# Kernel tuning notes

Hardware: AMD Instinct MI355X
Metric: run time of the kernel (lower is better)

The kernel has to match this reference:

```python
import jax, jax.numpy as jnp
import numpy as np

B, NX, NR, D, H = 8, 512, 512, 256, 256


def setup_inputs() -> dict:
    key = jax.random.key(0)
    ks = jax.random.split(key, 8)
    s = 1.0 / np.sqrt(D)
    sh = 1.0 / np.sqrt(H)
    return {
        "X": jax.random.normal(ks[0], (B, NX, D), dtype=jnp.float32),
        "ref": jax.random.normal(ks[1], (B, NR, D), dtype=jnp.float32),
        "W_X": jax.random.normal(ks[2], (H, D), dtype=jnp.float32) * s,
        "b_X": jax.random.normal(ks[3], (H,), dtype=jnp.float32) * s,
        "W_ref": jax.random.normal(ks[4], (H, D), dtype=jnp.float32) * s,
        "b_ref": jax.random.normal(ks[5], (H,), dtype=jnp.float32) * s,
        "v_w": jax.random.normal(ks[6], (1, H), dtype=jnp.float32) * sh,
        "v_b": jax.random.normal(ks[7], (1,), dtype=jnp.float32) * sh,
    }


def reference(X, ref, W_X, b_X, W_ref, b_ref, v_w, v_b):
    # linear projections: [B, nX, H], [B, nR, H]
    hX = jnp.einsum('bxd,hd->bxh', X, W_X) + b_X
    hR = jnp.einsum('brd,hd->brh', ref, W_ref) + b_ref
    # additive (Bahdanau) scores: [B, nX, nR]
    t = jnp.tanh(hX[:, :, None, :] + hR[:, None, :, :])
    out = jnp.einsum('bxrh,h->bxr', t, v_w[0]) + v_b[0]
    # softmax over the n_X axis (dim=1 in torch)
    attn = jax.nn.softmax(out, axis=1)
    # weighted sum of X per ref position: [B, nR, D]
    weighted_X = jnp.einsum('bxe,bxr->bre', X, attn)
    return weighted_X
```

## Files before the change

### kernel.cpp

```cpp
#include <hip/hip_runtime.h>
#include <math.h>

#define CB 8
#define CNX 512
#define CNR 512
#define CD 256
#define CH 256

typedef __attribute__((ext_vector_type(8))) short short8;
typedef __attribute__((ext_vector_type(4))) float f32x4;

__device__ __forceinline__ float fast_rcp(float x) {
#if __has_builtin(__builtin_amdgcn_rcpf)
  return __builtin_amdgcn_rcpf(x);
#else
  return 1.0f / x;
#endif
}
__device__ __forceinline__ float fast_exp2(float x) {
#if __has_builtin(__builtin_amdgcn_exp2f)
  return __builtin_amdgcn_exp2f(x);
#else
  return exp2f(x);
#endif
}

__device__ __forceinline__ void cvt_store(unsigned short* dstH,
                                          unsigned short* dstL,
                                          float4 v0, float4 v1) {
  unsigned u0x = __float_as_uint(v0.x), u0y = __float_as_uint(v0.y);
  unsigned u0z = __float_as_uint(v0.z), u0w = __float_as_uint(v0.w);
  unsigned u1x = __float_as_uint(v1.x), u1y = __float_as_uint(v1.y);
  unsigned u1z = __float_as_uint(v1.z), u1w = __float_as_uint(v1.w);
  uint4 H;
  H.x = (u0x >> 16) | (u0y & 0xFFFF0000u);
  H.y = (u0z >> 16) | (u0w & 0xFFFF0000u);
  H.z = (u1x >> 16) | (u1y & 0xFFFF0000u);
  H.w = (u1z >> 16) | (u1w & 0xFFFF0000u);
  float r0x = v0.x - __uint_as_float(u0x & 0xFFFF0000u);
  float r0y = v0.y - __uint_as_float(u0y & 0xFFFF0000u);
  float r0z = v0.z - __uint_as_float(u0z & 0xFFFF0000u);
  float r0w = v0.w - __uint_as_float(u0w & 0xFFFF0000u);
  float r1x = v1.x - __uint_as_float(u1x & 0xFFFF0000u);
  float r1y = v1.y - __uint_as_float(u1y & 0xFFFF0000u);
  float r1z = v1.z - __uint_as_float(u1z & 0xFFFF0000u);
  float r1w = v1.w - __uint_as_float(u1w & 0xFFFF0000u);
  uint4 L;
  L.x = (__float_as_uint(r0x) >> 16) | (__float_as_uint(r0y) & 0xFFFF0000u);
  L.y = (__float_as_uint(r0z) >> 16) | (__float_as_uint(r0w) & 0xFFFF0000u);
  L.z = (__float_as_uint(r1x) >> 16) | (__float_as_uint(r1y) & 0xFFFF0000u);
  L.w = (__float_as_uint(r1z) >> 16) | (__float_as_uint(r1w) & 0xFFFF0000u);
  *(uint4*)dstH = H;
  *(uint4*)dstL = L;
}

__device__ __forceinline__ void split4(float4 v, ushort4* H, ushort4* L) {
  unsigned ux = __float_as_uint(v.x), uy = __float_as_uint(v.y);
  unsigned uz = __float_as_uint(v.z), uw = __float_as_uint(v.w);
  H->x = (unsigned short)(ux >> 16);
  H->y = (unsigned short)(uy >> 16);
  H->z = (unsigned short)(uz >> 16);
  H->w = (unsigned short)(uw >> 16);
  float rx = v.x - __uint_as_float(ux & 0xFFFF0000u);
  float ry = v.y - __uint_as_float(uy & 0xFFFF0000u);
  float rz = v.z - __uint_as_float(uz & 0xFFFF0000u);
  float rw = v.w - __uint_as_float(uw & 0xFFFF0000u);
  L->x = (unsigned short)(__float_as_uint(rx) >> 16);
  L->y = (unsigned short)(__float_as_uint(ry) >> 16);
  L->z = (unsigned short)(__float_as_uint(rz) >> 16);
  L->w = (unsigned short)(__float_as_uint(rw) >> 16);
}

__global__ __launch_bounds__(256) void proj_mfma(
    const float* __restrict__ A0, const float* __restrict__ A1,
    const float* __restrict__ W0, const float* __restrict__ W1,
    const float* __restrict__ bias0, const float* __restrict__ bias1,
    float* __restrict__ E0, float* __restrict__ E1) {
  __shared__ unsigned short lds[2][4][64][40];
  const int K = CD;
  int z = blockIdx.z;
  const float* A = z ? A1 : A0;
  const float* W = z ? W1 : W0;
  const float* bias = z ? bias1 : bias0;
  float* ET = z ? E1 : E0;
  int m0 = blockIdx.x * 64, n0 = blockIdx.y * 64;
  int tid = threadIdx.x;
  int lane = tid & 63, w = tid >> 6;
  int wm = w >> 1, wn = w & 1;
  int r = tid >> 2, kq = (tid & 3) * 8;
  const float* pA = A + (size_t)(m0 + r) * K + kq;
  const float* pW = W + (size_t)(n0 + r) * K + kq;
  f32x4 acc[2][2] = {};
  float4 a0 = *(const float4*)(pA);
  float4 a1 = *(const float4*)(pA + 4);
  float4 w0 = *(const float4*)(pW);
  float4 w1 = *(const float4*)(pW + 4);
  cvt_store(&lds[0][0][r][kq], &lds[0][1][r][kq], a0, a1);
  cvt_store(&lds[0][2][r][kq], &lds[0][3][r][kq], w0, w1);
  for (int s = 0; s < 8; s++) {
    __syncthreads();
    if (s < 7) {
      int kt = (s + 1) * 32;
      a0 = *(const float4*)(pA + kt);
      a1 = *(const float4*)(pA + kt + 4);
      w0 = *(const float4*)(pW + kt);
      w1 = *(const float4*)(pW + kt + 4);
    }
    int cur = s & 1;
    int arow = wm * 32 + (lane & 15);
    int brow = wn * 32 + (lane & 15);
    int koff = (lane >> 4) * 8;
    short8 ah0 = *(const short8*)&lds[cur][0][arow][koff];
    short8 ah1 = *(const short8*)&lds[cur][0][arow + 16][koff];
    short8 al0 = *(const short8*)&lds[cur][1][arow][koff];
    short8 al1 = *(const short8*)&lds[cur][1][arow + 16][koff];
    short8 bh0 = *(const short8*)&lds[cur][2][brow][koff];
    short8 bh1 = *(const short8*)&lds[cur][2][brow + 16][koff];
    short8 bl0 = *(const short8*)&lds[cur][3][brow][koff];
    short8 bl1 = *(const short8*)&lds[cur][3][brow + 16][koff];
    acc[0][0] = __builtin_amdgcn_mfma_f32_16x16x32_bf16(ah0, bh0, acc[0][0], 0, 0, 0);
    acc[0][1] = __builtin_amdgcn_mfma_f32_16x16x32_bf16(ah0, bh1, acc[0][1], 0, 0, 0);
    acc[1][0] = __builtin_amdgcn_mfma_f32_16x16x32_bf16(ah1, bh0, acc[1][0], 0, 0, 0);
    acc[1][1] = __builtin_amdgcn_mfma_f32_16x16x32_bf16(ah1, bh1, acc[1][1], 0, 0, 0);
    acc[0][0] = __builtin_amdgcn_mfma_f32_16x16x32_bf16(ah0, bl0, acc[0][0], 0, 0, 0);
    acc[0][1] = __builtin_amdgcn_mfma_f32_16x16x32_bf16(ah0, bl1, acc[0][1], 0, 0, 0);
    acc[1][0] = __builtin_amdgcn_mfma_f32_16x16x32_bf16(ah1, bl0, acc[1][0], 0, 0, 0);
    acc[1][1] = __builtin_amdgcn_mfma_f32_16x16x32_bf16(ah1, bl1, acc[1][1], 0, 0, 0);
    acc[0][0] = __builtin_amdgcn_mfma_f32_16x16x32_bf16(al0, bh0, acc[0][0], 0, 0, 0);
    acc[0][1] = __builtin_amdgcn_mfma_f32_16x16x32_bf16(al0, bh1, acc[0][1], 0, 0, 0);
    acc[1][0] = __builtin_amdgcn_mfma_f32_16x16x32_bf16(al1, bh0, acc[1][0], 0, 0, 0);
    acc[1][1] = __builtin_amdgcn_mfma_f32_16x16x32_bf16(al1, bh1, acc[1][1], 0, 0, 0);
    if (s < 7) {
      int nxt = cur ^ 1;
      cvt_store(&lds[nxt][0][r][kq], &lds[nxt][1][r][kq], a0, a1);
      cvt_store(&lds[nxt][2][r][kq], &lds[nxt][3][r][kq], w0, w1);
    }
  }
  const float K2L = 2.8853900817779268f;
  int b = m0 >> 9;
  int xq = (m0 & 511) + wm * 32 + (lane >> 4) * 4;
#pragma unroll
  for (int mi = 0; mi < 2; mi++) {
#pragma unroll
    for (int ni = 0; ni < 2; ni++) {
      int h = n0 + wn * 32 + ni * 16 + (lane & 15);
      float bb = bias[h];
      f32x4 a = acc[mi][ni];
      float4 o = {fast_exp2(K2L * (a[0] + bb)), fast_exp2(K2L * (a[1] + bb)),
                  fast_exp2(K2L * (a[2] + bb)), fast_exp2(K2L * (a[3] + bb))};
      *(float4*)(ET + ((size_t)b * CH + h) * CNX + xq + mi * 16) = o;
    }
  }
}

__global__ __launch_bounds__(512) void scores_kernel(
    const float* __restrict__ exT, const float* __restrict__ erT,
    const float* __restrict__ v_w, float* __restrict__ scT) {
  __shared__ float smem[4 * 2048 + 256];
  int b = blockIdx.z;
  int x0 = blockIdx.x * 64, r0 = blockIdx.y * 64;
  int tid = threadIdx.x;
  int g = tid >> 8;
  int t = tid & 255;
  float* xs = smem + g * 4096;
  float* rs = xs + 2048;
  float* vsh = smem + 8192;
  if (tid < 256) vsh[tid] = v_w[tid];
  int tx = t & 15, ty = t >> 4;
  int sr = t >> 4, sc = (t & 15) * 4;
  int wrot = (tid >> 6) & 7;
  const float* pX = exT + (size_t)b * CH * CNX + x0 + sc;
  const float* pR = erT + (size_t)b * CH * CNR + r0 + sc;
  int hb = g * 32;
  float4 xa0 = *(const float4*)(pX + (size_t)(hb + sr) * CNX);
  float4 xa1 = *(const float4*)(pX + (size_t)(hb + sr + 16) * CNX);
  float4 ra0 = *(const float4*)(pR + (size_t)(hb + sr) * CNR);
  float4 ra1 = *(const float4*)(pR + (size_t)(hb + sr + 16) * CNR);
  float acc[4][4] = {};
  for (int hc = hb; hc < CH; hc += 64) {
    __syncthreads();
    *(float4*)&xs[sr * 64 + sc] = xa0;
    *(float4*)&xs[(sr + 16) * 64 + sc] = xa1;
    *(float4*)&rs[sr * 64 + sc] = ra0;
    *(float4*)&rs[(sr + 16) * 64 + sc] = ra1;
    __syncthreads();
    if (hc + 64 < CH) {
      xa0 = *(const float4*)(pX + (size_t)(hc + 64 + sr) * CNX);
      xa1 = *(const float4*)(pX + (size_t)(hc + 64 + sr + 16) * CNX);
      ra0 = *(const float4*)(pR + (size_t)(hc + 64 + sr) * CNR);
      ra1 = *(const float4*)(pR + (size_t)(hc + 64 + sr + 16) * CNR);
    }
#pragma unroll 2
    for (int hq = 0; hq < 8; hq++) {
      int h0 = ((hq + wrot) & 7) * 4;
      float4 vv = *(const float4*)&vsh[hc + h0];
      float4 xv0 = *(const float4*)&xs[(h0 + 0) * 64 + tx * 4];
      float4 xv1 = *(const float4*)&xs[(h0 + 1) * 64 + tx * 4];
      float4 xv2 = *(const float4*)&xs[(h0 + 2) * 64 + tx * 4];
      float4 xv3 = *(const float4*)&xs[(h0 + 3) * 64 + tx * 4];
      float4 rv0 = *(const float4*)&rs[(h0 + 0) * 64 + ty * 4];
      float4 rv1 = *(const float4*)&rs[(h0 + 1) * 64 + ty * 4];
      float4 rv2 = *(const float4*)&rs[(h0 + 2) * 64 + ty * 4];
      float4 rv3 = *(const float4*)&rs[(h0 + 3) * 64 + ty * 4];
      float xm0[4] = {xv0.x, xv0.y, xv0.z, xv0.w};
      float xm1[4] = {xv1.x, xv1.y, xv1.z, xv1.w};
      float xm2[4] = {xv2.x, xv2.y, xv2.z, xv2.w};
      float xm3[4] = {xv3.x, xv3.y, xv3.z, xv3.w};
      float rm0[4] = {rv0.x, rv0.y, rv0.z, rv0.w};
      float rm1[4] = {rv1.x, rv1.y, rv1.z, rv1.w};
      float rm2[4] = {rv2.x, rv2.y, rv2.z, rv2.w};
      float rm3[4] = {rv3.x, rv3.y, rv3.z, rv3.w};
#pragma unroll
      for (int i = 0; i < 4; i++)
#pragma unroll
        for (int j = 0; j < 4; j++) {
          float a = fmaf(rm0[i], xm0[j], 1.0f);
          float bb = fmaf(rm1[i], xm1[j], 1.0f);
          float c = fmaf(rm2[i], xm2[j], 1.0f);
          float d = fmaf(rm3[i], xm3[j], 1.0f);
          float q12 = a * bb, q34 = c * d;
          float p12 = fmaf(vv.y, a, vv.x * bb);
          float p34 = fmaf(vv.w, c, vv.z * d);
          float num = fmaf(p34, q12, p12 * q34);
          acc[i][j] = fmaf(num, fast_rcp(q12 * q34), acc[i][j]);
        }
    }
  }
  __syncthreads();
  float* mg = smem;
  if (g == 1) {
#pragma unroll
    for (int i = 0; i < 4; i++)
#pragma unroll
      for (int j = 0; j < 4; j++)
        mg[t + 256 * (i * 4 + j)] = acc[i][j];
  }
  __syncthreads();
  if (g == 0) {
    float* pO = scT + ((size_t)b * CNR + r0 + ty * 4) * CNX + x0 + tx * 4;
#pragma unroll
    for (int i = 0; i < 4; i++) {
      float4 o = {-2.0f * (acc[i][0] + mg[t + 256 * (i * 4 + 0)]),
                  -2.0f * (acc[i][1] + mg[t + 256 * (i * 4 + 1)]),
                  -2.0f * (acc[i][2] + mg[t + 256 * (i * 4 + 2)]),
                  -2.0f * (acc[i][3] + mg[t + 256 * (i * 4 + 3)])};
      *(float4*)(pO + (size_t)i * CNX) = o;
    }
  }
}

__global__ __launch_bounds__(512) void wsum_mfma(
    const float* __restrict__ scT, const float* __restrict__ X,
    float* __restrict__ out) {
  __shared__ unsigned short lds[2][2][64][64];
  __shared__ float dn[64];
  const float L2E = 1.4426950408889634f;
  int b = blockIdx.z;
  int r0 = blockIdx.x * 64, d0 = blockIdx.y * 64;
  int tid = threadIdx.x;
  int lane = tid & 63, w = tid >> 6;
  int wm = w >> 2, wn = w & 3;
  int pr = tid >> 3, pxk = (tid & 7) * 4;
  int psl = pxk >> 3, pof = pxk & 7;
  int xd = tid & 63, xx = (tid >> 6) * 4;
  int xsl = xx >> 3, xof = xx & 7;
  const float* pS = scT + ((size_t)b * CNR + r0 + pr) * CNX + pxk;
  const float* pX = X + ((size_t)b * CNX + xx) * CD + d0 + xd;
  f32x4 acc0 = {}, acc1 = {};
  float dsum = 0.0f;
  float4 sv = *(const float4*)(pS);
  float4 xv = {pX[0], pX[CD], pX[2 * CD], pX[3 * CD]};
  {
    float4 ev = {fast_exp2(sv.x * L2E), fast_exp2(sv.y * L2E),
                 fast_exp2(sv.z * L2E), fast_exp2(sv.w * L2E)};
    dsum += (ev.x + ev.y) + (ev.z + ev.w);
    ushort4 H, L;
    split4(ev, &H, &L);
    unsigned short* rp = &lds[0][0][pr][0];
    *(ushort4*)(rp + ((psl ^ (pr & 7)) << 3) + pof) = H;
    *(ushort4*)(rp + (((psl + 4) ^ (pr & 7)) << 3) + pof) = L;
    split4(xv, &H, &L);
    unsigned short* rx = &lds[0][1][xd][0];
    *(ushort4*)(rx + ((xsl ^ (xd & 7)) << 3) + xof) = H;
    *(ushort4*)(rx + (((xsl + 4) ^ (xd & 7)) << 3) + xof) = L;
  }
  int q = lane >> 4;
  int mr0 = wm * 32 + (lane & 15);
  int mr1 = mr0 + 16;
  int nr = wn * 16 + (lane & 15);
  for (int s = 0; s < 16; s++) {
    __syncthreads();
    if (s < 15) {
      int kt = (s + 1) * 32;
      sv = *(const float4*)(pS + kt);
      xv.x = pX[(size_t)(kt + 0) * CD];
      xv.y = pX[(size_t)(kt + 1) * CD];
      xv.z = pX[(size_t)(kt + 2) * CD];
      xv.w = pX[(size_t)(kt + 3) * CD];
    }
    int cur = s & 1;
    const unsigned short* Pt = &lds[cur][0][0][0];
    const unsigned short* Xt = &lds[cur][1][0][0];
    short8 ah0 = *(const short8*)(Pt + mr0 * 64 + ((q ^ (mr0 & 7)) << 3));
    short8 al0 = *(const short8*)(Pt + mr0 * 64 + (((q + 4) ^ (mr0 & 7)) << 3));
    short8 ah1 = *(const short8*)(Pt + mr1 * 64 + ((q ^ (mr1 & 7)) << 3));
    short8 al1 = *(const short8*)(Pt + mr1 * 64 + (((q + 4) ^ (mr1 & 7)) << 3));
    short8 bh = *(const short8*)(Xt + nr * 64 + ((q ^ (nr & 7)) << 3));
    short8 bl = *(const short8*)(Xt + nr * 64 + (((q + 4) ^ (nr & 7)) << 3));
    acc0 = __builtin_amdgcn_mfma_f32_16x16x32_bf16(ah0, bh, acc0, 0, 0, 0);
    acc1 = __builtin_amdgcn_mfma_f32_16x16x32_bf16(ah1, bh, acc1, 0, 0, 0);
    acc0 = __builtin_amdgcn_mfma_f32_16x16x32_bf16(ah0, bl, acc0, 0, 0, 0);
    acc1 = __builtin_amdgcn_mfma_f32_16x16x32_bf16(ah1, bl, acc1, 0, 0, 0);
    acc0 = __builtin_amdgcn_mfma_f32_16x16x32_bf16(al0, bh, acc0, 0, 0, 0);
    acc1 = __builtin_amdgcn_mfma_f32_16x16x32_bf16(al1, bh, acc1, 0, 0, 0);
    if (s < 15) {
      int nxt = cur ^ 1;
      float4 ev = {fast_exp2(sv.x * L2E), fast_exp2(sv.y * L2E),
                   fast_exp2(sv.z * L2E), fast_exp2(sv.w * L2E)};
      dsum += (ev.x + ev.y) + (ev.z + ev.w);
      ushort4 H, L;
      split4(ev, &H, &L);
      unsigned short* rp = &lds[nxt][0][pr][0];
      *(ushort4*)(rp + ((psl ^ (pr & 7)) << 3) + pof) = H;
      *(ushort4*)(rp + (((psl + 4) ^ (pr & 7)) << 3) + pof) = L;
      split4(xv, &H, &L);
      unsigned short* rx = &lds[nxt][1][xd][0];
      *(ushort4*)(rx + ((xsl ^ (xd & 7)) << 3) + xof) = H;
      *(ushort4*)(rx + (((xsl + 4) ^ (xd & 7)) << 3) + xof) = L;
    }
  }
  dsum += __shfl_xor(dsum, 1, 64);
  dsum += __shfl_xor(dsum, 2, 64);
  dsum += __shfl_xor(dsum, 4, 64);
  if ((tid & 7) == 0) dn[pr] = dsum;
  __syncthreads();
  int col = d0 + wn * 16 + (lane & 15);
  float* pO = out + ((size_t)b * CNR + r0) * CD + col;
#pragma unroll
  for (int j = 0; j < 4; j++) {
    int row = wm * 32 + q * 4 + j;
    pO[(size_t)row * CD] = acc0[j] * fast_rcp(dn[row]);
  }
#pragma unroll
  for (int j = 0; j < 4; j++) {
    int row = wm * 32 + 16 + q * 4 + j;
    pO[(size_t)row * CD] = acc1[j] * fast_rcp(dn[row]);
  }
}

extern "C" void kernel_launch(void* const* d_in, const int* in_sizes, int n_in,
                              void* d_out, int out_size, void* d_ws, size_t ws_size,
                              hipStream_t stream) {
  const float* X     = (const float*)d_in[0];
  const float* ref   = (const float*)d_in[1];
  const float* W_X   = (const float*)d_in[2];
  const float* b_X   = (const float*)d_in[3];
  const float* W_ref = (const float*)d_in[4];
  const float* b_ref = (const float*)d_in[5];
  const float* v_w   = (const float*)d_in[6];
  float* out = (float*)d_out;
  float* ws  = (float*)d_ws;

  float* exT = ws;
  float* erT = ws + 1048576;
  float* scT = ws + 2097152;

  proj_mfma<<<dim3(64, 4, 2), 256, 0, stream>>>(X, ref, W_X, W_ref, b_X, b_ref, exT, erT);
  scores_kernel<<<dim3(8, 8, 8), 512, 0, stream>>>(exT, erT, v_w, scT);
  wsum_mfma<<<dim3(8, 4, 8), 512, 0, stream>>>(scT, X, out);
}
```

Before: 132.8 us.

## Restructure scores kernel: 4-way H split, 4x8 tiles, double-buffered LDS

The scores kernel now uses 256-thread blocks over 64x32 output tiles. Each of four waves handles a different slice of H, and each thread computes a 4x8 sub-tile instead of 4x4. The H chunks are double-buffered in LDS with a register prefetch, so there is one barrier per chunk instead of two. The wave partial sums are combined through a swizzled two-level LDS reduction. The aim is more register reuse per LDS load and better latency hiding, at the cost of more accumulator registers and extra reduction steps.

```diff
diff --git a/kernel.cpp b/kernel.cpp
--- a/kernel.cpp
+++ b/kernel.cpp
@@ -69,6 +69,31 @@
   L->y = (unsigned short)(__float_as_uint(ry) >> 16);
   L->z = (unsigned short)(__float_as_uint(rz) >> 16);
   L->w = (unsigned short)(__float_as_uint(rw) >> 16);
+}
+
+__device__ __forceinline__ void merge_wr(float* buf, int lane,
+                                         const float a[4][8]) {
+#pragma unroll
+  for (int i = 0; i < 4; i++) {
+    int s0 = ((2 * i) ^ (lane & 7)) << 2;
+    int s1 = ((2 * i + 1) ^ (lane & 7)) << 2;
+    float4 v0 = {a[i][0], a[i][1], a[i][2], a[i][3]};
+    float4 v1 = {a[i][4], a[i][5], a[i][6], a[i][7]};
+    *(float4*)&buf[lane * 32 + s0] = v0;
+    *(float4*)&buf[lane * 32 + s1] = v1;
+  }
+}
+__device__ __forceinline__ void merge_rd(const float* buf, int lane,
+                                         float a[4][8]) {
+#pragma unroll
+  for (int i = 0; i < 4; i++) {
+    int s0 = ((2 * i) ^ (lane & 7)) << 2;
+    int s1 = ((2 * i + 1) ^ (lane & 7)) << 2;
+    float4 v0 = *(const float4*)&buf[lane * 32 + s0];
+    float4 v1 = *(const float4*)&buf[lane * 32 + s1];
+    a[i][0] += v0.x; a[i][1] += v0.y; a[i][2] += v0.z; a[i][3] += v0.w;
+    a[i][4] += v1.x; a[i][5] += v1.y; a[i][6] += v1.z; a[i][7] += v1.w;
+  }
 }
 
 __global__ __launch_bounds__(256) void proj_mfma(
@@ -153,98 +178,104 @@
   }
 }
 
-__global__ __launch_bounds__(512) void scores_kernel(
+__global__ __launch_bounds__(256, 4) void scores_kernel(
     const float* __restrict__ exT, const float* __restrict__ erT,
     const float* __restrict__ v_w, float* __restrict__ scT) {
-  __shared__ float smem[4 * 2048 + 256];
+  __shared__ float smem[6144 + 256];
   int b = blockIdx.z;
-  int x0 = blockIdx.x * 64, r0 = blockIdx.y * 64;
+  int x0 = blockIdx.x * 64, r0 = blockIdx.y * 32;
   int tid = threadIdx.x;
-  int g = tid >> 8;
-  int t = tid & 255;
-  float* xs = smem + g * 4096;
-  float* rs = xs + 2048;
-  float* vsh = smem + 8192;
-  if (tid < 256) vsh[tid] = v_w[tid];
-  int tx = t & 15, ty = t >> 4;
-  int sr = t >> 4, sc = (t & 15) * 4;
-  int wrot = (tid >> 6) & 7;
-  const float* pX = exT + (size_t)b * CH * CNX + x0 + sc;
-  const float* pR = erT + (size_t)b * CH * CNR + r0 + sc;
-  int hb = g * 32;
-  float4 xa0 = *(const float4*)(pX + (size_t)(hb + sr) * CNX);
-  float4 xa1 = *(const float4*)(pX + (size_t)(hb + sr + 16) * CNX);
-  float4 ra0 = *(const float4*)(pR + (size_t)(hb + sr) * CNR);
-  float4 ra1 = *(const float4*)(pR + (size_t)(hb + sr + 16) * CNR);
-  float acc[4][4] = {};
-  for (int hc = hb; hc < CH; hc += 64) {
+  int lane = tid & 63, g = tid >> 6;
+  int tx = lane & 7, ty = lane >> 3;
+  float* vsh = smem + 6144;
+  vsh[tid] = v_w[tid];
+  int srow = tid >> 3, sxc = (tid & 7) * 8, src = (tid & 7) * 4;
+  const float* pX = exT + (size_t)b * CH * CNX + x0;
+  const float* pR = erT + (size_t)b * CH * CNR + r0;
+  float4 px0 = *(const float4*)(pX + (size_t)srow * CNX + sxc);
+  float4 px1 = *(const float4*)(pX + (size_t)srow * CNX + sxc + 4);
+  float4 pr0 = *(const float4*)(pR + (size_t)srow * CNR + src);
+  {
+    float* xs = smem;
+    float* rs = smem + 2048;
+    *(float4*)&xs[srow * 64 + sxc] = px0;
+    *(float4*)&xs[srow * 64 + sxc + 4] = px1;
+    *(float4*)&rs[srow * 32 + src] = pr0;
+  }
+  float acc[4][8] = {};
+  for (int c = 0; c < 8; c++) {
     __syncthreads();
-    *(float4*)&xs[sr * 64 + sc] = xa0;
-    *(float4*)&xs[(sr + 16) * 64 + sc] = xa1;
-    *(float4*)&rs[sr * 64 + sc] = ra0;
-    *(float4*)&rs[(sr + 16) * 64 + sc] = ra1;
-    __syncthreads();
-    if (hc + 64 < CH) {
-      xa0 = *(const float4*)(pX + (size_t)(hc + 64 + sr) * CNX);
-      xa1 = *(const float4*)(pX + (size_t)(hc + 64 + sr + 16) * CNX);
-      ra0 = *(const float4*)(pR + (size_t)(hc + 64 + sr) * CNR);
-      ra1 = *(const float4*)(pR + (size_t)(hc + 64 + sr + 16) * CNR);
-    }
-#pragma unroll 2
-    for (int hq = 0; hq < 8; hq++) {
-      int h0 = ((hq + wrot) & 7) * 4;
-      float4 vv = *(const float4*)&vsh[hc + h0];
-      float4 xv0 = *(const float4*)&xs[(h0 + 0) * 64 + tx * 4];
-      float4 xv1 = *(const float4*)&xs[(h0 + 1) * 64 + tx * 4];
-      float4 xv2 = *(const float4*)&xs[(h0 + 2) * 64 + tx * 4];
-      float4 xv3 = *(const float4*)&xs[(h0 + 3) * 64 + tx * 4];
-      float4 rv0 = *(const float4*)&rs[(h0 + 0) * 64 + ty * 4];
-      float4 rv1 = *(const float4*)&rs[(h0 + 1) * 64 + ty * 4];
-      float4 rv2 = *(const float4*)&rs[(h0 + 2) * 64 + ty * 4];
-      float4 rv3 = *(const float4*)&rs[(h0 + 3) * 64 + ty * 4];
-      float xm0[4] = {xv0.x, xv0.y, xv0.z, xv0.w};
-      float xm1[4] = {xv1.x, xv1.y, xv1.z, xv1.w};
-      float xm2[4] = {xv2.x, xv2.y, xv2.z, xv2.w};
-      float xm3[4] = {xv3.x, xv3.y, xv3.z, xv3.w};
-      float rm0[4] = {rv0.x, rv0.y, rv0.z, rv0.w};
-      float rm1[4] = {rv1.x, rv1.y, rv1.z, rv1.w};
-      float rm2[4] = {rv2.x, rv2.y, rv2.z, rv2.w};
-      float rm3[4] = {rv3.x, rv3.y, rv3.z, rv3.w};
+    if (c < 7) {
+      int hn = (c + 1) * 32 + srow;
+      px0 = *(const float4*)(pX + (size_t)hn * CNX + sxc);
+      px1 = *(const float4*)(pX + (size_t)hn * CNX + sxc + 4);
+      pr0 = *(const float4*)(pR + (size_t)hn * CNR + src);
+    }
+    const float* xs = smem + (c & 1) * 3072;
+    const float* rs = xs + 2048;
+#pragma unroll
+    for (int q = 0; q < 2; q++) {
+      int hl = g * 8 + q * 4;
+      float4 vv = *(const float4*)&vsh[c * 32 + hl];
+      float xm0[8], xm1[8], xm2[8], xm3[8];
+      float rm0[4], rm1[4], rm2[4], rm3[4];
+      *(float4*)&xm0[0] = *(const float4*)&xs[(hl + 0) * 64 + tx * 8];
+      *(float4*)&xm0[4] = *(const float4*)&xs[(hl + 0) * 64 + tx * 8 + 4];
+      *(float4*)&xm1[0] = *(const float4*)&xs[(hl + 1) * 64 + tx * 8];
+      *(float4*)&xm1[4] = *(const float4*)&xs[(hl + 1) * 64 + tx * 8 + 4];
+      *(float4*)&xm2[0] = *(const float4*)&xs[(hl + 2) * 64 + tx * 8];
+      *(float4*)&xm2[4] = *(const float4*)&xs[(hl + 2) * 64 + tx * 8 + 4];
+      *(float4*)&xm3[0] = *(const float4*)&xs[(hl + 3) * 64 + tx * 8];
+      *(float4*)&xm3[4] = *(const float4*)&xs[(hl + 3) * 64 + tx * 8 + 4];
+      *(float4*)&rm0[0] = *(const float4*)&rs[(hl + 0) * 32 + ty * 4];
+      *(float4*)&rm1[0] = *(const float4*)&rs[(hl + 1) * 32 + ty * 4];
+      *(float4*)&rm2[0] = *(const float4*)&rs[(hl + 2) * 32 + ty * 4];
+      *(float4*)&rm3[0] = *(const float4*)&rs[(hl + 3) * 32 + ty * 4];
 #pragma unroll
       for (int i = 0; i < 4; i++)
 #pragma unroll
-        for (int j = 0; j < 4; j++) {
+        for (int j = 0; j < 8; j++) {
           float a = fmaf(rm0[i], xm0[j], 1.0f);
           float bb = fmaf(rm1[i], xm1[j], 1.0f);
-          float c = fmaf(rm2[i], xm2[j], 1.0f);
-          float d = fmaf(rm3[i], xm3[j], 1.0f);
-          float q12 = a * bb, q34 = c * d;
+          float cc = fmaf(rm2[i], xm2[j], 1.0f);
+          float dd = fmaf(rm3[i], xm3[j], 1.0f);
+          float q12 = a * bb, q34 = cc * dd;
           float p12 = fmaf(vv.y, a, vv.x * bb);
-          float p34 = fmaf(vv.w, c, vv.z * d);
+          float p34 = fmaf(vv.w, cc, vv.z * dd);
           float num = fmaf(p34, q12, p12 * q34);
           acc[i][j] = fmaf(num, fast_rcp(q12 * q34), acc[i][j]);
         }
     }
-  }
+    if (c < 7) {
+      float* xw = smem + ((c + 1) & 1) * 3072;
+      float* rw = xw + 2048;
+      *(float4*)&xw[srow * 64 + sxc] = px0;
+      *(float4*)&xw[srow * 64 + sxc + 4] = px1;
+      *(float4*)&rw[srow * 32 + src] = pr0;
+    }
+  }
+  float* bufA = smem;
+  float* bufB = smem + 2048;
   __syncthreads();
-  float* mg = smem;
-  if (g == 1) {
-#pragma unroll
-    for (int i = 0; i < 4; i++)
-#pragma unroll
-      for (int j = 0; j < 4; j++)
-        mg[t + 256 * (i * 4 + j)] = acc[i][j];
-  }
+  if (g == 1) merge_wr(bufA, lane, acc);
+  if (g == 3) merge_wr(bufB, lane, acc);
+  __syncthreads();
+  if (g == 0) merge_rd(bufA, lane, acc);
+  if (g == 2) merge_rd(bufB, lane, acc);
+  __syncthreads();
+  if (g == 2) merge_wr(bufA, lane, acc);
   __syncthreads();
   if (g == 0) {
-    float* pO = scT + ((size_t)b * CNR + r0 + ty * 4) * CNX + x0 + tx * 4;
+    merge_rd(bufA, lane, acc);
+    float* pO = scT + ((size_t)b * CNR + r0 + ty * 4) * CNX + x0 + tx * 8;
 #pragma unroll
     for (int i = 0; i < 4; i++) {
-      float4 o = {-2.0f * (acc[i][0] + mg[t + 256 * (i * 4 + 0)]),
-                  -2.0f * (acc[i][1] + mg[t + 256 * (i * 4 + 1)]),
-                  -2.0f * (acc[i][2] + mg[t + 256 * (i * 4 + 2)]),
-                  -2.0f * (acc[i][3] + mg[t + 256 * (i * 4 + 3)])};
-      *(float4*)(pO + (size_t)i * CNX) = o;
+      float4 o0 = {-2.0f * acc[i][0], -2.0f * acc[i][1],
+                   -2.0f * acc[i][2], -2.0f * acc[i][3]};
+      float4 o1 = {-2.0f * acc[i][4], -2.0f * acc[i][5],
+                   -2.0f * acc[i][6], -2.0f * acc[i][7]};
+      *(float4*)(pO + (size_t)i * CNX) = o0;
+      *(float4*)(pO + (size_t)i * CNX + 4) = o1;
     }
   }
 }
@@ -366,6 +397,6 @@
   float* scT = ws + 2097152;
 
   proj_mfma<<<dim3(64, 4, 2), 256, 0, stream>>>(X, ref, W_X, W_ref, b_X, b_ref, exT, erT);
-  scores_kernel<<<dim3(8, 8, 8), 512, 0, stream>>>(exT, erT, v_w, scT);
+  scores_kernel<<<dim3(8, 16, 8), 256, 0, stream>>>(exT, erT, v_w, scT);
   wsum_mfma<<<dim3(8, 4, 8), 512, 0, stream>>>(scT, X, out);
 }
```

After: 240.1 us. 80.7% more time.

## Precompute bf16 hi/lo splits of scores and X; drop LDS staging in GEMMs

Applied to the files above, without the earlier changes.

The projection GEMM now loads fp32 operands straight from global memory into registers in MFMA fragment layout and splits them to bf16 hi/lo there, removing the LDS double buffer and its barriers. The scores kernel applies exp and writes bf16 hi/lo probability planes instead of fp32 scores. A new kernel transposes X and splits it into bf16 hi/lo planes, so the weighted-sum kernel becomes a barrier-free MFMA loop over pre-split global data with smaller tiles, and it computes the softmax denominator from the split values. This adds a kernel launch and extra global traffic in exchange for less LDS and conversion work inside the hot loops. Reusing the exT workspace region for XH/XL is safe only because the scores kernel finishes reading it before xt_kernel runs.

```diff
diff --git a/kernel.cpp b/kernel.cpp
--- a/kernel.cpp
+++ b/kernel.cpp
@@ -9,6 +9,7 @@
 
 typedef __attribute__((ext_vector_type(8))) short short8;
 typedef __attribute__((ext_vector_type(4))) float f32x4;
+typedef __attribute__((ext_vector_type(4))) unsigned int uint32x4;
 
 __device__ __forceinline__ float fast_rcp(float x) {
 #if __has_builtin(__builtin_amdgcn_rcpf)
@@ -25,33 +26,29 @@
 #endif
 }
 
-__device__ __forceinline__ void cvt_store(unsigned short* dstH,
-                                          unsigned short* dstL,
-                                          float4 v0, float4 v1) {
-  unsigned u0x = __float_as_uint(v0.x), u0y = __float_as_uint(v0.y);
-  unsigned u0z = __float_as_uint(v0.z), u0w = __float_as_uint(v0.w);
-  unsigned u1x = __float_as_uint(v1.x), u1y = __float_as_uint(v1.y);
-  unsigned u1z = __float_as_uint(v1.z), u1w = __float_as_uint(v1.w);
-  uint4 H;
-  H.x = (u0x >> 16) | (u0y & 0xFFFF0000u);
-  H.y = (u0z >> 16) | (u0w & 0xFFFF0000u);
-  H.z = (u1x >> 16) | (u1y & 0xFFFF0000u);
-  H.w = (u1z >> 16) | (u1w & 0xFFFF0000u);
-  float r0x = v0.x - __uint_as_float(u0x & 0xFFFF0000u);
-  float r0y = v0.y - __uint_as_float(u0y & 0xFFFF0000u);
-  float r0z = v0.z - __uint_as_float(u0z & 0xFFFF0000u);
-  float r0w = v0.w - __uint_as_float(u0w & 0xFFFF0000u);
-  float r1x = v1.x - __uint_as_float(u1x & 0xFFFF0000u);
-  float r1y = v1.y - __uint_as_float(u1y & 0xFFFF0000u);
-  float r1z = v1.z - __uint_as_float(u1z & 0xFFFF0000u);
-  float r1w = v1.w - __uint_as_float(u1w & 0xFFFF0000u);
-  uint4 L;
-  L.x = (__float_as_uint(r0x) >> 16) | (__float_as_uint(r0y) & 0xFFFF0000u);
-  L.y = (__float_as_uint(r0z) >> 16) | (__float_as_uint(r0w) & 0xFFFF0000u);
-  L.z = (__float_as_uint(r1x) >> 16) | (__float_as_uint(r1y) & 0xFFFF0000u);
-  L.w = (__float_as_uint(r1z) >> 16) | (__float_as_uint(r1w) & 0xFFFF0000u);
-  *(uint4*)dstH = H;
-  *(uint4*)dstL = L;
+__device__ __forceinline__ void split8(float4 u, float4 v, short8* H, short8* L) {
+  unsigned ux = __float_as_uint(u.x), uy = __float_as_uint(u.y);
+  unsigned uz = __float_as_uint(u.z), uw = __float_as_uint(u.w);
+  unsigned vx = __float_as_uint(v.x), vy = __float_as_uint(v.y);
+  unsigned vz = __float_as_uint(v.z), vw = __float_as_uint(v.w);
+  uint32x4 Hp = {(ux >> 16) | (uy & 0xFFFF0000u),
+                 (uz >> 16) | (uw & 0xFFFF0000u),
+                 (vx >> 16) | (vy & 0xFFFF0000u),
+                 (vz >> 16) | (vw & 0xFFFF0000u)};
+  float rux = u.x - __uint_as_float(ux & 0xFFFF0000u);
+  float ruy = u.y - __uint_as_float(uy & 0xFFFF0000u);
+  float ruz = u.z - __uint_as_float(uz & 0xFFFF0000u);
+  float ruw = u.w - __uint_as_float(uw & 0xFFFF0000u);
+  float rvx = v.x - __uint_as_float(vx & 0xFFFF0000u);
+  float rvy = v.y - __uint_as_float(vy & 0xFFFF0000u);
+  float rvz = v.z - __uint_as_float(vz & 0xFFFF0000u);
+  float rvw = v.w - __uint_as_float(vw & 0xFFFF0000u);
+  uint32x4 Lp = {(__float_as_uint(rux) >> 16) | (__float_as_uint(ruy) & 0xFFFF0000u),
+                 (__float_as_uint(ruz) >> 16) | (__float_as_uint(ruw) & 0xFFFF0000u),
+                 (__float_as_uint(rvx) >> 16) | (__float_as_uint(rvy) & 0xFFFF0000u),
+                 (__float_as_uint(rvz) >> 16) | (__float_as_uint(rvw) & 0xFFFF0000u)};
+  *H = __builtin_bit_cast(short8, Hp);
+  *L = __builtin_bit_cast(short8, Lp);
 }
 
 __device__ __forceinline__ void split4(float4 v, ushort4* H, ushort4* L) {
@@ -76,8 +73,6 @@
     const float* __restrict__ W0, const float* __restrict__ W1,
     const float* __restrict__ bias0, const float* __restrict__ bias1,
     float* __restrict__ E0, float* __restrict__ E1) {
-  __shared__ unsigned short lds[2][4][64][40];
-  const int K = CD;
   int z = blockIdx.z;
   const float* A = z ? A1 : A0;
   const float* W = z ? W1 : W0;
@@ -87,37 +82,25 @@
   int tid = threadIdx.x;
   int lane = tid & 63, w = tid >> 6;
   int wm = w >> 1, wn = w & 1;
-  int r = tid >> 2, kq = (tid & 3) * 8;
-  const float* pA = A + (size_t)(m0 + r) * K + kq;
-  const float* pW = W + (size_t)(n0 + r) * K + kq;
+  int q = lane >> 4, ml = lane & 15;
+  const float* pA = A + (size_t)(m0 + wm * 32 + ml) * CD + q * 8;
+  const float* pW = W + (size_t)(n0 + wn * 32 + ml) * CD + q * 8;
   f32x4 acc[2][2] = {};
-  float4 a0 = *(const float4*)(pA);
-  float4 a1 = *(const float4*)(pA + 4);
-  float4 w0 = *(const float4*)(pW);
-  float4 w1 = *(const float4*)(pW + 4);
-  cvt_store(&lds[0][0][r][kq], &lds[0][1][r][kq], a0, a1);
-  cvt_store(&lds[0][2][r][kq], &lds[0][3][r][kq], w0, w1);
   for (int s = 0; s < 8; s++) {
-    __syncthreads();
-    if (s < 7) {
-      int kt = (s + 1) * 32;
-      a0 = *(const float4*)(pA + kt);
-      a1 = *(const float4*)(pA + kt + 4);
-      w0 = *(const float4*)(pW + kt);
-      w1 = *(const float4*)(pW + kt + 4);
-    }
-    int cur = s & 1;
-    int arow = wm * 32 + (lane & 15);
-    int brow = wn * 32 + (lane & 15);
-    int koff = (lane >> 4) * 8;
-    short8 ah0 = *(const short8*)&lds[cur][0][arow][koff];
-    short8 ah1 = *(const short8*)&lds[cur][0][arow + 16][koff];
-    short8 al0 = *(const short8*)&lds[cur][1][arow][koff];
-    short8 al1 = *(const short8*)&lds[cur][1][arow + 16][koff];
-    short8 bh0 = *(const short8*)&lds[cur][2][brow][koff];
-    short8 bh1 = *(const short8*)&lds[cur][2][brow + 16][koff];
-    short8 bl0 = *(const short8*)&lds[cur][3][brow][koff];
-    short8 bl1 = *(const short8*)&lds[cur][3][brow + 16][koff];
+    int kt = s * 32;
+    float4 a0a = *(const float4*)(pA + kt);
+    float4 a0b = *(const float4*)(pA + kt + 4);
+    float4 a1a = *(const float4*)(pA + 16 * CD + kt);
+    float4 a1b = *(const float4*)(pA + 16 * CD + kt + 4);
+    float4 w0a = *(const float4*)(pW + kt);
+    float4 w0b = *(const float4*)(pW + kt + 4);
+    float4 w1a = *(const float4*)(pW + 16 * CD + kt);
+    float4 w1b = *(const float4*)(pW + 16 * CD + kt + 4);
+    short8 ah0, al0, ah1, al1, bh0, bl0, bh1, bl1;
+    split8(a0a, a0b, &ah0, &al0);
+    split8(a1a, a1b, &ah1, &al1);
+    split8(w0a, w0b, &bh0, &bl0);
+    split8(w1a, w1b, &bh1, &bl1);
     acc[0][0] = __builtin_amdgcn_mfma_f32_16x16x32_bf16(ah0, bh0, acc[0][0], 0, 0, 0);
     acc[0][1] = __builtin_amdgcn_mfma_f32_16x16x32_bf16(ah0, bh1, acc[0][1], 0, 0, 0);
     acc[1][0] = __builtin_amdgcn_mfma_f32_16x16x32_bf16(ah1, bh0, acc[1][0], 0, 0, 0);
@@ -130,20 +113,15 @@
     acc[0][1] = __builtin_amdgcn_mfma_f32_16x16x32_bf16(al0, bh1, acc[0][1], 0, 0, 0);
     acc[1][0] = __builtin_amdgcn_mfma_f32_16x16x32_bf16(al1, bh0, acc[1][0], 0, 0, 0);
     acc[1][1] = __builtin_amdgcn_mfma_f32_16x16x32_bf16(al1, bh1, acc[1][1], 0, 0, 0);
-    if (s < 7) {
-      int nxt = cur ^ 1;
-      cvt_store(&lds[nxt][0][r][kq], &lds[nxt][1][r][kq], a0, a1);
-      cvt_store(&lds[nxt][2][r][kq], &lds[nxt][3][r][kq], w0, w1);
-    }
   }
   const float K2L = 2.8853900817779268f;
   int b = m0 >> 9;
-  int xq = (m0 & 511) + wm * 32 + (lane >> 4) * 4;
+  int xq = (m0 & 511) + wm * 32 + q * 4;
 #pragma unroll
   for (int mi = 0; mi < 2; mi++) {
 #pragma unroll
     for (int ni = 0; ni < 2; ni++) {
-      int h = n0 + wn * 32 + ni * 16 + (lane & 15);
+      int h = n0 + wn * 32 + ni * 16 + ml;
       float bb = bias[h];
       f32x4 a = acc[mi][ni];
       float4 o = {fast_exp2(K2L * (a[0] + bb)), fast_exp2(K2L * (a[1] + bb)),
@@ -155,7 +133,8 @@
 
 __global__ __launch_bounds__(512) void scores_kernel(
     const float* __restrict__ exT, const float* __restrict__ erT,
-    const float* __restrict__ v_w, float* __restrict__ scT) {
+    const float* __restrict__ v_w,
+    unsigned short* __restrict__ PH, unsigned short* __restrict__ PL) {
   __shared__ float smem[4 * 2048 + 256];
   int b = blockIdx.z;
   int x0 = blockIdx.x * 64, r0 = blockIdx.y * 64;
@@ -237,113 +216,124 @@
   }
   __syncthreads();
   if (g == 0) {
-    float* pO = scT + ((size_t)b * CNR + r0 + ty * 4) * CNX + x0 + tx * 4;
+    const float L2E = 1.4426950408889634f;
+    size_t ro = ((size_t)b * CNR + r0 + ty * 4) * CNX + x0 + tx * 4;
 #pragma unroll
     for (int i = 0; i < 4; i++) {
-      float4 o = {-2.0f * (acc[i][0] + mg[t + 256 * (i * 4 + 0)]),
-                  -2.0f * (acc[i][1] + mg[t + 256 * (i * 4 + 1)]),
-                  -2.0f * (acc[i][2] + mg[t + 256 * (i * 4 + 2)]),
-                  -2.0f * (acc[i][3] + mg[t + 256 * (i * 4 + 3)])};
-      *(float4*)(pO + (size_t)i * CNX) = o;
-    }
-  }
-}
-
-__global__ __launch_bounds__(512) void wsum_mfma(
-    const float* __restrict__ scT, const float* __restrict__ X,
+      float4 sv = {-2.0f * (acc[i][0] + mg[t + 256 * (i * 4 + 0)]),
+                   -2.0f * (acc[i][1] + mg[t + 256 * (i * 4 + 1)]),
+                   -2.0f * (acc[i][2] + mg[t + 256 * (i * 4 + 2)]),
+                   -2.0f * (acc[i][3] + mg[t + 256 * (i * 4 + 3)])};
+      float4 pv = {fast_exp2(sv.x * L2E), fast_exp2(sv.y * L2E),
+                   fast_exp2(sv.z * L2E), fast_exp2(sv.w * L2E)};
+      ushort4 H, L;
+      split4(pv, &H, &L);
+      *(ushort4*)(PH + ro + (size_t)i * CNX) = H;
+      *(ushort4*)(PL + ro + (size_t)i * CNX) = L;
+    }
+  }
+}
+
+__global__ __launch_bounds__(256) void xt_kernel(
+    const float* __restrict__ X,
+    unsigned short* __restrict__ XH, unsigned short* __restrict__ XL) {
+  __shared__ float T[64][68];
+  int b = blockIdx.z;
+  int x0 = blockIdx.x * 64, d0 = blockIdx.y * 64;
+  int t = threadIdx.x;
+  int xl = t >> 4, c4 = (t & 15) * 4;
+#pragma unroll
+  for (int p = 0; p < 4; p++) {
+    float4 v = *(const float4*)(X + ((size_t)(b * 512 + x0 + xl + p * 16)) * CD + d0 + c4);
+    *(float4*)&T[xl + p * 16][c4] = v;
+  }
+  __syncthreads();
+  int dl = t & 63, xseg = t >> 6;
+  unsigned h[8], l[8];
+#pragma unroll
+  for (int i = 0; i < 8; i++) {
+    float f0 = T[xseg * 16 + 2 * i][dl];
+    float f1 = T[xseg * 16 + 2 * i + 1][dl];
+    unsigned u0 = __float_as_uint(f0), u1 = __float_as_uint(f1);
+    h[i] = (u0 >> 16) | (u1 & 0xFFFF0000u);
+    float r0 = f0 - __uint_as_float(u0 & 0xFFFF0000u);
+    float r1 = f1 - __uint_as_float(u1 & 0xFFFF0000u);
+    l[i] = (__float_as_uint(r0) >> 16) | (__float_as_uint(r1) & 0xFFFF0000u);
+  }
+  size_t o = ((size_t)(b * 256 + d0 + dl)) * CNX + x0 + xseg * 16;
+  uint4 h0 = {h[0], h[1], h[2], h[3]};
+  uint4 h1 = {h[4], h[5], h[6], h[7]};
+  uint4 l0 = {l[0], l[1], l[2], l[3]};
+  uint4 l1 = {l[4], l[5], l[6], l[7]};
+  *(uint4*)(XH + o) = h0;
+  *(uint4*)(XH + o + 8) = h1;
+  *(uint4*)(XL + o) = l0;
+  *(uint4*)(XL + o + 8) = l1;
+}
+
+__global__ __launch_bounds__(256) void wsum_mfma(
+    const unsigned short* __restrict__ PH, const unsigned short* __restrict__ PL,
+    const unsigned short* __restrict__ XH, const unsigned short* __restrict__ XL,
     float* __restrict__ out) {
-  __shared__ unsigned short lds[2][2][64][64];
-  __shared__ float dn[64];
-  const float L2E = 1.4426950408889634f;
+  __shared__ float dn[32];
   int b = blockIdx.z;
-  int r0 = blockIdx.x * 64, d0 = blockIdx.y * 64;
+  int r0 = blockIdx.x * 32, d0 = blockIdx.y * 64;
   int tid = threadIdx.x;
-  int lane = tid & 63, w = tid >> 6;
-  int wm = w >> 2, wn = w & 3;
-  int pr = tid >> 3, pxk = (tid & 7) * 4;
-  int psl = pxk >> 3, pof = pxk & 7;
-  int xd = tid & 63, xx = (tid >> 6) * 4;
-  int xsl = xx >> 3, xof = xx & 7;
-  const float* pS = scT + ((size_t)b * CNR + r0 + pr) * CNX + pxk;
-  const float* pX = X + ((size_t)b * CNX + xx) * CD + d0 + xd;
+  int lane = tid & 63, wn = tid >> 6;
+  int q = lane >> 4, ml = lane & 15;
+  const unsigned short* pPh = PH + ((size_t)b * CNR + r0 + ml) * CNX + q * 8;
+  const unsigned short* pPl = PL + ((size_t)b * CNR + r0 + ml) * CNX + q * 8;
+  const unsigned short* pXh = XH + ((size_t)b * CD + d0 + wn * 16 + ml) * CNX + q * 8;
+  const unsigned short* pXl = XL + ((size_t)b * CD + d0 + wn * 16 + ml) * CNX + q * 8;
   f32x4 acc0 = {}, acc1 = {};
-  float dsum = 0.0f;
-  float4 sv = *(const float4*)(pS);
-  float4 xv = {pX[0], pX[CD], pX[2 * CD], pX[3 * CD]};
-  {
-    float4 ev = {fast_exp2(sv.x * L2E), fast_exp2(sv.y * L2E),
-                 fast_exp2(sv.z * L2E), fast_exp2(sv.w * L2E)};
-    dsum += (ev.x + ev.y) + (ev.z + ev.w);
-    ushort4 H, L;
-    split4(ev, &H, &L);
-    unsigned short* rp = &lds[0][0][pr][0];
-    *(ushort4*)(rp + ((psl ^ (pr & 7)) << 3) + pof) = H;
-    *(ushort4*)(rp + (((psl + 4) ^ (pr & 7)) << 3) + pof) = L;
-    split4(xv, &H, &L);
-    unsigned short* rx = &lds[0][1][xd][0];
-    *(ushort4*)(rx + ((xsl ^ (xd & 7)) << 3) + xof) = H;
-    *(ushort4*)(rx + (((xsl + 4) ^ (xd & 7)) << 3) + xof) = L;
-  }
-  int q = lane >> 4;
-  int mr0 = wm * 32 + (lane & 15);
-  int mr1 = mr0 + 16;
-  int nr = wn * 16 + (lane & 15);
+  float d0s = 0.0f, d1s = 0.0f;
   for (int s = 0; s < 16; s++) {
-    __syncthreads();
-    if (s < 15) {
-      int kt = (s + 1) * 32;
-      sv = *(const float4*)(pS + kt);
-      xv.x = pX[(size_t)(kt + 0) * CD];
-      xv.y = pX[(size_t)(kt + 1) * CD];
-      xv.z = pX[(size_t)(kt + 2) * CD];
-      xv.w = pX[(size_t)(kt + 3) * CD];
-    }
-    int cur = s & 1;
-    const unsigned short* Pt = &lds[cur][0][0][0];
-    const unsigned short* Xt = &lds[cur][1][0][0];
-    short8 ah0 = *(const short8*)(Pt + mr0 * 64 + ((q ^ (mr0 & 7)) << 3));
-    short8 al0 = *(const short8*)(Pt + mr0 * 64 + (((q + 4) ^ (mr0 & 7)) << 3));
-    short8 ah1 = *(const short8*)(Pt + mr1 * 64 + ((q ^ (mr1 & 7)) << 3));
-    short8 al1 = *(const short8*)(Pt + mr1 * 64 + (((q + 4) ^ (mr1 & 7)) << 3));
-    short8 bh = *(const short8*)(Xt + nr * 64 + ((q ^ (nr & 7)) << 3));
-    short8 bl = *(const short8*)(Xt + nr * 64 + (((q + 4) ^ (nr & 7)) << 3));
+    int kt = s * 32;
+    short8 ah0 = *(const short8*)(pPh + kt);
+    short8 ah1 = *(const short8*)(pPh + kt + 16 * CNX);
+    short8 al0 = *(const short8*)(pPl + kt);
+    short8 al1 = *(const short8*)(pPl + kt + 16 * CNX);
+    short8 bh = *(const short8*)(pXh + kt);
+    short8 bl = *(const short8*)(pXl + kt);
     acc0 = __builtin_amdgcn_mfma_f32_16x16x32_bf16(ah0, bh, acc0, 0, 0, 0);
     acc1 = __builtin_amdgcn_mfma_f32_16x16x32_bf16(ah1, bh, acc1, 0, 0, 0);
     acc0 = __builtin_amdgcn_mfma_f32_16x16x32_bf16(ah0, bl, acc0, 0, 0, 0);
     acc1 = __builtin_amdgcn_mfma_f32_16x16x32_bf16(ah1, bl, acc1, 0, 0, 0);
     acc0 = __builtin_amdgcn_mfma_f32_16x16x32_bf16(al0, bh, acc0, 0, 0, 0);
     acc1 = __builtin_amdgcn_mfma_f32_16x16x32_bf16(al1, bh, acc1, 0, 0, 0);
-    if (s < 15) {
-      int nxt = cur ^ 1;
-      float4 ev = {fast_exp2(sv.x * L2E), fast_exp2(sv.y * L2E),
-                   fast_exp2(sv.z * L2E), fast_exp2(sv.w * L2E)};
-      dsum += (ev.x + ev.y) + (ev.z + ev.w);
-      ushort4 H, L;
-      split4(ev, &H, &L);
-      unsigned short* rp = &lds[nxt][0][pr][0];
-      *(ushort4*)(rp + ((psl ^ (pr & 7)) << 3) + pof) = H;
-      *(ushort4*)(rp + (((psl + 4) ^ (pr & 7)) << 3) + pof) = L;
-      split4(xv, &H, &L);
-      unsigned short* rx = &lds[nxt][1][xd][0];
-      *(ushort4*)(rx + ((xsl ^ (xd & 7)) << 3) + xof) = H;
-      *(ushort4*)(rx + (((xsl + 4) ^ (xd & 7)) << 3) + xof) = L;
-    }
-  }
-  dsum += __shfl_xor(dsum, 1, 64);
-  dsum += __shfl_xor(dsum, 2, 64);
-  dsum += __shfl_xor(dsum, 4, 64);
-  if ((tid & 7) == 0) dn[pr] = dsum;
+    if (wn == 0) {
+#pragma unroll
+      for (int j = 0; j < 8; j++) {
+        float p0 = __uint_as_float(((unsigned)(unsigned short)ah0[j]) << 16) +
+                   __uint_as_float(((unsigned)(unsigned short)al0[j]) << 16);
+        float p1 = __uint_as_float(((unsigned)(unsigned short)ah1[j]) << 16) +
+                   __uint_as_float(((unsigned)(unsigned short)al1[j]) << 16);
+        d0s += p0;
+        d1s += p1;
+      }
+    }
+  }
+  if (wn == 0) {
+    d0s += __shfl_xor(d0s, 16, 64);
+    d0s += __shfl_xor(d0s, 32, 64);
+    d1s += __shfl_xor(d1s, 16, 64);
+    d1s += __shfl_xor(d1s, 32, 64);
+    if (lane < 16) {
+      dn[lane] = d0s;
+      dn[16 + lane] = d1s;
+    }
+  }
   __syncthreads();
-  int col = d0 + wn * 16 + (lane & 15);
+  int col = d0 + wn * 16 + ml;
   float* pO = out + ((size_t)b * CNR + r0) * CD + col;
 #pragma unroll
   for (int j = 0; j < 4; j++) {
-    int row = wm * 32 + q * 4 + j;
+    int row = q * 4 + j;
     pO[(size_t)row * CD] = acc0[j] * fast_rcp(dn[row]);
   }
 #pragma unroll
   for (int j = 0; j < 4; j++) {
-    int row = wm * 32 + 16 + q * 4 + j;
+    int row = 16 + q * 4 + j;
     pO[(size_t)row * CD] = acc1[j] * fast_rcp(dn[row]);
   }
 }
@@ -363,9 +353,13 @@
 
   float* exT = ws;
   float* erT = ws + 1048576;
-  float* scT = ws + 2097152;
+  unsigned short* PH = (unsigned short*)(ws + 2097152);
+  unsigned short* PL = PH + 2097152;
+  unsigned short* XH = (unsigned short*)ws;
+  unsigned short* XL = XH + 1048576;
 
   proj_mfma<<<dim3(64, 4, 2), 256, 0, stream>>>(X, ref, W_X, W_ref, b_X, b_ref, exT, erT);
-  scores_kernel<<<dim3(8, 8, 8), 512, 0, stream>>>(exT, erT, v_w, scT);
-  wsum_mfma<<<dim3(8, 4, 8), 512, 0, stream>>>(scT, X, out);
-}
+  scores_kernel<<<dim3(8, 8, 8), 512, 0, stream>>>(exT, erT, v_w, PH, PL);
+  xt_kernel<<<dim3(8, 4, 8), 256, 0, stream>>>(X, XH, XL);
+  wsum_mfma<<<dim3(16, 4, 8), 256, 0, stream>>>(PH, PL, XH, XL, out);
+}
```

New measurement: 157.1 us. 1.18x slower.
